# Kernel optimization log

Hardware: AMD Instinct MI355X
Metric: run time of the kernel (lower is better)

Reference implementation:

```python
import jax, jax.numpy as jnp
from jax import lax
import numpy as np

G = 33            # LUT grid size per axis (hard-coded in module)
G3 = G * G * G    # 35937 entries per channel LUT


def _gelu(x):
    return jax.nn.gelu(x, approximate=False)  # torch nn.GELU default = exact erf


def _conv(x, w, b):
    # 3x3 stride-1 padding-1 conv == SAME padding, NCHW/OIHW like torch
    y = lax.conv_general_dilated(x, w, (1, 1), 'SAME',
                                 dimension_numbers=('NCHW', 'OIHW', 'NCHW'))
    return y + b[None, :, None, None]


def _bn(x, g, b, eps=1e-5):
    # eval-mode BatchNorm2d with running_mean=0, running_var=1
    s = g * (1.0 + eps) ** -0.5
    return x * s[None, :, None, None] + b[None, :, None, None]


def _resblock(x, wA, bA, gA, btA, wB, bB, gB, btB):
    h = _gelu(_bn(_conv(x, wA, bA), gA, btA))
    h = _bn(_conv(h, wB, bB), gB, btB)
    return _gelu(h + x)


def _apply_luts(luts_flat, recon):
    # Trilinear 3D-LUT sampling == F.grid_sample(mode='bilinear', padding_mode='border',
    # align_corners=True) on a 5D LUT. grid = recon[...,[2,1,0]]*2-1 means image ch0 (R)
    # indexes LUT dim 2, ch1 (G) dim 3, ch2 (B) dim 4; align_corners maps v->v*(G-1).
    # luts_flat: [B, L*3, G^3] (all num_luts fused into the channel dim, gathered once)
    # recon:     [B, 3, H, W] in [0,1]
    B, C3, _ = luts_flat.shape
    _, _, H, W = recon.shape
    c = jnp.clip(recon * (G - 1.0), 0.0, G - 1.0)      # border clamp
    f0 = jnp.clip(jnp.floor(c), 0.0, G - 2.0)
    t = c - f0                                          # fractional weights [B,3,H,W]
    i0 = f0.astype(jnp.int32)
    r0, g0, b0 = i0[:, 0], i0[:, 1], i0[:, 2]           # [B,H,W] each
    tr, tg, tb = t[:, 0], t[:, 1], t[:, 2]
    out = jnp.zeros((B, C3, H * W), dtype=luts_flat.dtype)
    for dr in (0, 1):
        for dg in (0, 1):
            for db in (0, 1):
                idx = ((r0 + dr) * G + (g0 + dg)) * G + (b0 + db)   # [B,H,W]
                w = ((tr if dr else 1.0 - tr) * (tg if dg else 1.0 - tg)
                     * (tb if db else 1.0 - tb))
                vals = jnp.take_along_axis(luts_flat, idx.reshape(B, 1, H * W), axis=2)
                out = out + vals * w.reshape(B, 1, H * W)
    return out.reshape(B, C3 // 3, 3, H, W)            # [B, L, 3, H, W]


def setup_inputs() -> dict:
    key = jax.random.key(0)
    ks = iter(jax.random.split(key, 32))
    def nrm(shape, s=0.02):
        return jax.random.normal(next(ks), shape, jnp.float32) * s
    B, T, V, E, HID, L, H, W = 4, 1024, 1024, 256, 256, 8, 384, 384
    inp = dict(
        tokens=jax.random.randint(next(ks), (B, T), 0, V),
        img=jax.random.uniform(next(ks), (B, 3, H, W), jnp.float32),
        recon_image=jax.random.uniform(next(ks), (B, 3, H, W), jnp.float32),
        emb_table=nrm((V, E)),
        agg_w1=nrm((E, HID)), agg_b1=jnp.zeros((HID,), jnp.float32),
        agg_w2=nrm((HID, HID)), agg_b2=jnp.zeros((HID,), jnp.float32),
        lut_w1=nrm((HID, HID)), lut_b1=jnp.zeros((HID,), jnp.float32),
        lut_w2=nrm((HID, L * 3 * G3), 0.005),
        lut_b2=jnp.zeros((L * 3 * G3,), jnp.float32),
        wg_w1=nrm((HID, HID // 4)), wg_b1=jnp.zeros((HID // 4,), jnp.float32),
        wg_w2=nrm((HID // 4, L)), wg_b2=jnp.zeros((L,), jnp.float32),
        rp_cin_w=nrm((32, 3, 3, 3)), rp_cin_b=jnp.zeros((32,), jnp.float32),
        rp_rbA_w=nrm((32, 32, 3, 3)), rp_rbA_b=jnp.zeros((32,), jnp.float32),
        rp_rbA_g=jnp.ones((32,), jnp.float32), rp_rbA_bt=jnp.zeros((32,), jnp.float32),
        rp_rbB_w=nrm((32, 32, 3, 3)), rp_rbB_b=jnp.zeros((32,), jnp.float32),
        rp_rbB_g=jnp.ones((32,), jnp.float32), rp_rbB_bt=jnp.zeros((32,), jnp.float32),
        rp_cout_w=nrm((3, 32, 3, 3)), rp_cout_b=jnp.zeros((3,), jnp.float32),
        fu_cin_w=nrm((32, 6, 3, 3)), fu_cin_b=jnp.zeros((32,), jnp.float32),
        fu_rbA_w=nrm((32, 32, 3, 3)), fu_rbA_b=jnp.zeros((32,), jnp.float32),
        fu_rbA_g=jnp.ones((32,), jnp.float32), fu_rbA_bt=jnp.zeros((32,), jnp.float32),
        fu_rbB_w=nrm((32, 32, 3, 3)), fu_rbB_b=jnp.zeros((32,), jnp.float32),
        fu_rbB_g=jnp.ones((32,), jnp.float32), fu_rbB_bt=jnp.zeros((32,), jnp.float32),
        fu_cout_w=nrm((3, 32, 3, 3)), fu_cout_b=jnp.zeros((3,), jnp.float32),
    )
    return inp


def reference(tokens, img, recon_image, emb_table,
              agg_w1, agg_b1, agg_w2, agg_b2,
              lut_w1, lut_b1, lut_w2, lut_b2,
              wg_w1, wg_b1, wg_w2, wg_b2,
              rp_cin_w, rp_cin_b, rp_rbA_w, rp_rbA_b, rp_rbA_g, rp_rbA_bt,
              rp_rbB_w, rp_rbB_b, rp_rbB_g, rp_rbB_bt, rp_cout_w, rp_cout_b,
              fu_cin_w, fu_cin_b, fu_rbA_w, fu_rbA_b, fu_rbA_g, fu_rbA_bt,
              fu_rbB_w, fu_rbB_b, fu_rbB_g, fu_rbB_bt, fu_cout_w, fu_cout_b):
    B = img.shape[0]
    L = wg_w2.shape[1]
    # token features
    emb = emb_table[tokens]                       # [B, T, E]
    tf = jnp.mean(emb, axis=1)                    # [B, E]
    tf = _gelu(tf @ agg_w1 + agg_b1) @ agg_w2 + agg_b2   # [B, HID]
    # dynamic LUTs and fusion weights
    lut_params = _gelu(tf @ lut_w1 + lut_b1) @ lut_w2 + lut_b2   # [B, L*3*G3]
    luts_flat = lut_params.reshape(B, L * 3, G3)
    lw = jax.nn.softmax(_gelu(tf @ wg_w1 + wg_b1) @ wg_w2 + wg_b2, axis=1)  # [B, L]
    # apply all LUTs in one fused gather pass, then weighted sum over LUTs
    lut_out = _apply_luts(luts_flat, recon_image)                # [B, L, 3, H, W]
    fused = jnp.einsum('blchw,bl->bchw', lut_out, lw)            # [B, 3, H, W]
    # residual processing branch on original img
    proc = _gelu(_conv(img, rp_cin_w, rp_cin_b))
    proc = _resblock(proc, rp_rbA_w, rp_rbA_b, rp_rbA_g, rp_rbA_bt,
                     rp_rbB_w, rp_rbB_b, rp_rbB_g, rp_rbB_bt)
    proc = _conv(proc, rp_cout_w, rp_cout_b)
    # fusion
    comb = jnp.concatenate([fused, proc], axis=1)                # [B, 6, H, W]
    out = _gelu(_conv(comb, fu_cin_w, fu_cin_b))
    out = _resblock(out, fu_rbA_w, fu_rbA_b, fu_rbA_g, fu_rbA_bt,
                    fu_rbB_w, fu_rbB_b, fu_rbB_g, fu_rbB_bt)
    out = _conv(out, fu_cout_w, fu_cout_b)
    return out + img
```

## Files before the change

### kernel.cpp

```cpp
#include <hip/hip_runtime.h>
#include <hip/hip_bf16.h>
#include <math.h>

#define BB    4
#define TT    1024
#define EE    256
#define HIDD  256
#define LLUT  8
#define HGT   384
#define WID   384
#define HWPX  147456
#define GSZ   33
#define G3    35937
#define NCOL  862488

typedef __attribute__((ext_vector_type(8))) short bf16x8;
typedef __attribute__((ext_vector_type(4))) float f32x4;

__device__ __forceinline__ float gelu_f(float x) {
    float s = 1.5957691216057308f * x * (1.0f + 0.044715f * x * x);
    float e = __expf(s);
    return x - x / (e + 1.0f);
}

__device__ __forceinline__ ushort f2bf(float x) {
    uint u = __float_as_uint(x);
    return (ushort)((u + 0x7FFFu + ((u >> 16) & 1u)) >> 16);
}
__device__ __forceinline__ uint pack2bf(float a, float b) {
    return (uint)f2bf(a) | ((uint)f2bf(b) << 16);
}
__device__ __forceinline__ float bf2f_lo(uint u) { return __uint_as_float(u << 16); }
__device__ __forceinline__ float bf2f_hi(uint u) { return __uint_as_float(u & 0xFFFF0000u); }

__global__ __launch_bounds__(256) void emb_partial_kernel(
    const int* __restrict__ tokens, const float* __restrict__ emb,
    float* __restrict__ partial)
{
    const int s = blockIdx.x, b = blockIdx.y, tid = threadIdx.x;
    const int* tok = tokens + b * TT + s * 16;
    float acc = 0.f;
#pragma unroll
    for (int t = 0; t < 16; ++t) acc += emb[tok[t] * EE + tid];
    partial[(b * 64 + s) * EE + tid] = acc;
}

__global__ __launch_bounds__(1024) void mlp_head_kernel(
    const float* __restrict__ partial,
    const float* __restrict__ aw1, const float* __restrict__ ab1,
    const float* __restrict__ aw2, const float* __restrict__ ab2,
    const float* __restrict__ lw1, const float* __restrict__ lb1,
    const float* __restrict__ gw1, const float* __restrict__ gb1,
    const float* __restrict__ gw2, const float* __restrict__ gb2,
    float* __restrict__ h3_out, float* __restrict__ lw_out)
{
    const int b = blockIdx.x;
    const int tid = threadIdx.x;
    const int o = tid & 255;
    const int q = tid >> 8;
    __shared__ float tf[256], h1[256], tf2s[256], h4[64], lg[8];
    __shared__ float red[4][256];

    {
        float acc = 0.f;
#pragma unroll
        for (int s = 0; s < 16; ++s)
            acc += partial[(b * 64 + q * 16 + s) * EE + o];
        red[q][o] = acc;
    }
    __syncthreads();
    if (tid < 256)
        tf[tid] = (red[0][tid] + red[1][tid] + red[2][tid] + red[3][tid]) * (1.0f / TT);
    __syncthreads();

    {
        float s = 0.f;
#pragma unroll 8
        for (int j = 0; j < 64; ++j) {
            const int k = (q << 6) + j;
            s += tf[k] * aw1[k * HIDD + o];
        }
        red[q][o] = s;
    }
    __syncthreads();
    if (tid < 256)
        h1[tid] = gelu_f(red[0][tid] + red[1][tid] + red[2][tid] + red[3][tid] + ab1[tid]);
    __syncthreads();

    {
        float s = 0.f;
#pragma unroll 8
        for (int j = 0; j < 64; ++j) {
            const int k = (q << 6) + j;
            s += h1[k] * aw2[k * HIDD + o];
        }
        red[q][o] = s;
    }
    __syncthreads();
    if (tid < 256)
        tf2s[tid] = red[0][tid] + red[1][tid] + red[2][tid] + red[3][tid] + ab2[tid];
    __syncthreads();

    {
        float s = 0.f;
#pragma unroll 8
        for (int j = 0; j < 64; ++j) {
            const int k = (q << 6) + j;
            s += tf2s[k] * lw1[k * HIDD + o];
        }
        red[q][o] = s;
    }
    __syncthreads();
    if (tid < 256)
        h3_out[b * HIDD + tid] =
            gelu_f(red[0][tid] + red[1][tid] + red[2][tid] + red[3][tid] + lb1[tid]);
    __syncthreads();

    {
        const int o64 = tid & 63, q16 = tid >> 6;
        float s = 0.f;
#pragma unroll
        for (int j = 0; j < 16; ++j) {
            const int k = q16 * 16 + j;
            s += tf2s[k] * gw1[k * 64 + o64];
        }
        ((float*)red)[q16 * 64 + o64] = s;
    }
    __syncthreads();
    if (tid < 64) {
        float s = gb1[tid];
#pragma unroll
        for (int r = 0; r < 16; ++r) s += ((float*)red)[r * 64 + tid];
        h4[tid] = gelu_f(s);
    }
    __syncthreads();

    if (tid < 8) {
        float s = gb2[tid];
#pragma unroll 8
        for (int k = 0; k < 64; ++k) s += h4[k] * gw2[k * LLUT + tid];
        lg[tid] = s;
    }
    __syncthreads();
    if (tid == 0) {
        float m = lg[0];
        for (int i = 1; i < LLUT; ++i) m = fmaxf(m, lg[i]);
        float ssum = 0.f, ex[LLUT];
        for (int i = 0; i < LLUT; ++i) { ex[i] = expf(lg[i] - m); ssum += ex[i]; }
        for (int i = 0; i < LLUT; ++i) lw_out[b * LLUT + i] = ex[i] / ssum;
    }
}

__global__ __launch_bounds__(256) void lut_fused_kernel(
    const float* __restrict__ h3, const float* __restrict__ lwv,
    const float* __restrict__ w2, const float* __restrict__ b2,
    float* __restrict__ clut)
{
    __shared__ float h[BB * HIDD];
    __shared__ float lws[BB * LLUT];
    const int tid = threadIdx.x;
    for (int i = tid; i < BB * HIDD; i += 256) h[i] = h3[i];
    if (tid < BB * LLUT) lws[tid] = lwv[tid];
    __syncthreads();

    const int idx = blockIdx.x * 256 + tid;
    if (idx >= 3 * G3) return;
    const int c = idx / G3, v = idx - c * G3;

    float acc[BB][LLUT];
#pragma unroll
    for (int b = 0; b < BB; ++b)
#pragma unroll
        for (int l = 0; l < LLUT; ++l) acc[b][l] = 0.f;

    const float* wbase = w2 + (long)c * G3 + v;
#pragma unroll 4
    for (int k = 0; k < HIDD; ++k) {
        const float* row = wbase + (long)k * NCOL;
        float wl[LLUT];
#pragma unroll
        for (int l = 0; l < LLUT; ++l) wl[l] = row[l * 3 * G3];
#pragma unroll
        for (int b = 0; b < BB; ++b) {
            const float hb = h[b * HIDD + k];
#pragma unroll
            for (int l = 0; l < LLUT; ++l) acc[b][l] += wl[l] * hb;
        }
    }

    float bb[LLUT];
#pragma unroll
    for (int l = 0; l < LLUT; ++l) bb[l] = b2[(long)(l * 3 + c) * G3 + v];

#pragma unroll
    for (int b = 0; b < BB; ++b) {
        float s = 0.f;
#pragma unroll
        for (int l = 0; l < LLUT; ++l) s += lws[b * LLUT + l] * (acc[b][l] + bb[l]);
        clut[(long)(b * 3 + c) * G3 + v] = s;
    }
}

__global__ __launch_bounds__(256) void applylut_out3_kernel(
    const float* __restrict__ clut, const float* __restrict__ recon,
    const ushort* __restrict__ act2, const float* __restrict__ wgt,
    const float* __restrict__ bias, float* __restrict__ comb)
{
    const int p = blockIdx.x * 256 + threadIdx.x;
    const int b = blockIdx.y;

    const float* rc = recon + (long)b * 3 * HWPX;
    float cr = fminf(fmaxf(rc[p] * 32.f, 0.f), 32.f);
    float cg = fminf(fmaxf(rc[HWPX + p] * 32.f, 0.f), 32.f);
    float cb = fminf(fmaxf(rc[2 * HWPX + p] * 32.f, 0.f), 32.f);
    float fr = fminf(floorf(cr), 31.f);
    float fg = fminf(floorf(cg), 31.f);
    float fb = fminf(floorf(cb), 31.f);
    float tr = cr - fr, tg = cg - fg, tb_ = cb - fb;
    int idx = (((int)fr * GSZ + (int)fg) * GSZ + (int)fb);
    float c[3];
#pragma unroll
    for (int ch = 0; ch < 3; ++ch) {
        const float* lut = clut + (long)(b * 3 + ch) * G3;
        float v000 = lut[idx],                  v001 = lut[idx + 1];
        float v010 = lut[idx + GSZ],            v011 = lut[idx + GSZ + 1];
        float v100 = lut[idx + GSZ * GSZ],      v101 = lut[idx + GSZ * GSZ + 1];
        float v110 = lut[idx + GSZ * GSZ + GSZ], v111 = lut[idx + GSZ * GSZ + GSZ + 1];
        float c00 = v000 + (v001 - v000) * tb_;
        float c01 = v010 + (v011 - v010) * tb_;
        float c10 = v100 + (v101 - v100) * tb_;
        float c11 = v110 + (v111 - v110) * tb_;
        float c0 = c00 + (c01 - c00) * tg;
        float c1 = c10 + (c11 - c10) * tg;
        c[ch] = c0 + (c1 - c0) * tr;
    }
    float4 r4; r4.x = c[0]; r4.y = c[1]; r4.z = c[2]; r4.w = 0.f;
    *(float4*)(comb + ((long)b * HWPX + p) * 8) = r4;

    const int hh = p / WID, ww = p - hh * WID;
    float acc[3] = {bias[0], bias[1], bias[2]};
#pragma unroll
    for (int tap = 0; tap < 9; ++tap) {
        const int dh = tap / 3, dw = tap - dh * 3;
        const int gh = hh + dh - 1, gw = ww + dw - 1;
        if (gh < 0 || gh >= HGT || gw < 0 || gw >= WID) continue;
        const uint4* xp = (const uint4*)(act2 + ((long)b * HWPX + gh * WID + gw) * 32);
        float xx[32];
#pragma unroll
        for (int q = 0; q < 4; ++q) {
            uint4 v = xp[q];
            xx[q * 8 + 0] = bf2f_lo(v.x); xx[q * 8 + 1] = bf2f_hi(v.x);
            xx[q * 8 + 2] = bf2f_lo(v.y); xx[q * 8 + 3] = bf2f_hi(v.y);
            xx[q * 8 + 4] = bf2f_lo(v.z); xx[q * 8 + 5] = bf2f_hi(v.z);
            xx[q * 8 + 6] = bf2f_lo(v.w); xx[q * 8 + 7] = bf2f_hi(v.w);
        }
#pragma unroll
        for (int o = 0; o < 3; ++o)
#pragma unroll
            for (int ci = 0; ci < 32; ++ci)
                acc[o] += xx[ci] * wgt[o * 288 + ci * 9 + tap];
    }
    float4 s4; s4.x = acc[0]; s4.y = acc[1]; s4.z = acc[2]; s4.w = 0.f;
    *(float4*)(comb + ((long)b * HWPX + p) * 8 + 4) = s4;
}

__global__ __launch_bounds__(256) void conv_in3_kernel(
    const float* __restrict__ img, const float* __restrict__ wgt,
    const float* __restrict__ bias, ushort* __restrict__ out)
{
    const int tid = threadIdx.x;
    const int p0 = (blockIdx.x * 256 + tid) * 2;
    const int b = blockIdx.y;
    const int hh = p0 / WID, ww = p0 - hh * WID;

    float acc[32][2];
#pragma unroll
    for (int o = 0; o < 32; ++o) { float bv = bias[o]; acc[o][0] = bv; acc[o][1] = bv; }

    const bool wlo = (ww > 0), whi = (ww + 2 < WID);
#pragma unroll
    for (int ci = 0; ci < 3; ++ci) {
        const float* ip = img + (long)(b * 3 + ci) * HWPX;
        float x[3][4];
#pragma unroll
        for (int dh = 0; dh < 3; ++dh) {
            const int hs = hh + dh - 1;
            const bool hok = (hs >= 0) && (hs < HGT);
            const float* rp_ = ip + hs * WID + ww;
            x[dh][0] = (hok && wlo) ? rp_[-1] : 0.f;
            x[dh][1] = hok ? rp_[0] : 0.f;
            x[dh][2] = hok ? rp_[1] : 0.f;
            x[dh][3] = (hok && whi) ? rp_[2] : 0.f;
        }
#pragma unroll
        for (int o = 0; o < 32; ++o) {
            const float* wv = wgt + o * 27 + ci * 9;
#pragma unroll
            for (int dh = 0; dh < 3; ++dh)
#pragma unroll
                for (int dw = 0; dw < 3; ++dw) {
                    const float w = wv[dh * 3 + dw];
                    acc[o][0] += x[dh][dw]     * w;
                    acc[o][1] += x[dh][dw + 1] * w;
                }
        }
    }

    ushort* op = out + ((long)b * HWPX + p0) * 32;
#pragma unroll
    for (int px = 0; px < 2; ++px) {
        uint u[16];
#pragma unroll
        for (int o2 = 0; o2 < 16; ++o2)
            u[o2] = pack2bf(gelu_f(acc[2 * o2][px]), gelu_f(acc[2 * o2 + 1][px]));
        uint4* dst = (uint4*)(op + px * 32);
#pragma unroll
        for (int q = 0; q < 4; ++q)
            dst[q] = make_uint4(u[4 * q], u[4 * q + 1], u[4 * q + 2], u[4 * q + 3]);
    }
}

#define TH2 8
#define TW2 64
#define NTX (WID / TW2)
#define NTY (HGT / TH2)
#define NBLK (NTX * NTY * BB)
#define CHUNK (NBLK / 8)
#define HALO_H2 10
#define HALO_W2 66
#define CSTR 40

template <bool HAS_RES>
__global__ __launch_bounds__(512, 4) void conv32_mfma(
    const ushort* __restrict__ in, const ushort* __restrict__ res,
    const float* __restrict__ wgt, const float* __restrict__ bias,
    const float* __restrict__ bn_g, const float* __restrict__ bn_bt,
    ushort* __restrict__ out)
{
    __shared__ ushort halo[HALO_H2 * HALO_W2 * CSTR];
    __shared__ ushort wlA[9 * 2 * 64 * 8];
    __shared__ float s_scale[32], s_shift[32];

    const int tid = threadIdx.x;
    const int bid = blockIdx.x;
    const int t   = (bid & 7) * CHUNK + (bid >> 3);
    const int tx  = t % NTX;
    const int rem = t / NTX;
    const int ty  = rem % NTY;
    const int b   = rem / NTY;
    const int h0 = ty * TH2;
    const int w0 = tx * TW2;

    for (int i = tid; i < 9 * 2 * 64 * 8; i += 512) {
        const int j    = i & 7;
        const int lane_= (i >> 3) & 63;
        const int half = (i >> 9) & 1;
        const int tap  = i >> 10;
        const int co = half * 16 + (lane_ & 15);
        const int ci = (lane_ >> 4) * 8 + j;
        wlA[i] = f2bf(wgt[co * 288 + ci * 9 + tap]);
    }
    if (tid < 32) {
        float sg = bn_g[tid] * 0.9999950000375f;
        s_scale[tid] = sg;
        s_shift[tid] = bias[tid] * sg + bn_bt[tid];
    }

    const ushort* inb = in + (long)b * HWPX * 32;
    for (int i = tid; i < HALO_H2 * HALO_W2 * 4; i += 512) {
        const int row = i / (HALO_W2 * 4);
        const int rem2 = i - row * (HALO_W2 * 4);
        const int px = rem2 >> 2, q = rem2 & 3;
        const int gh = h0 + row - 1, gw = w0 + px - 1;
        uint4 v = make_uint4(0u, 0u, 0u, 0u);
        if (gh >= 0 && gh < HGT && gw >= 0 && gw < WID)
            v = *(const uint4*)(inb + ((long)gh * WID + gw) * 32 + q * 8);
        *(uint4*)(&halo[(row * HALO_W2 + px) * CSTR + q * 8]) = v;
    }
    __syncthreads();

    const int lane = tid & 63, wid = tid >> 6;
    const int l15 = lane & 15, kg = lane >> 4;
    const int r = wid;

    f32x4 acc[4][2];
#pragma unroll
    for (int f = 0; f < 4; ++f)
#pragma unroll
        for (int cf = 0; cf < 2; ++cf)
            acc[f][cf] = (f32x4){0.f, 0.f, 0.f, 0.f};

#pragma unroll
    for (int tap = 0; tap < 9; ++tap) {
        const int dh = tap / 3, dw = tap - dh * 3;
        const bf16x8 a0 = *(const bf16x8*)(&wlA[((tap * 2 + 0) * 64 + lane) * 8]);
        const bf16x8 a1 = *(const bf16x8*)(&wlA[((tap * 2 + 1) * 64 + lane) * 8]);
#pragma unroll
        for (int f = 0; f < 4; ++f) {
            const int c0 = f * 16;
            const bf16x8 bfv = *(const bf16x8*)(
                &halo[((r + dh) * HALO_W2 + (c0 + dw + l15)) * CSTR + kg * 8]);
            acc[f][0] = __builtin_amdgcn_mfma_f32_16x16x32_bf16(a0, bfv, acc[f][0], 0, 0, 0);
            acc[f][1] = __builtin_amdgcn_mfma_f32_16x16x32_bf16(a1, bfv, acc[f][1], 0, 0, 0);
        }
    }

#pragma unroll
    for (int f = 0; f < 4; ++f) {
        const int c0 = f * 16;
        const long gpx = (long)b * HWPX + (long)(h0 + r) * WID + (w0 + c0 + l15);
#pragma unroll
        for (int cf = 0; cf < 2; ++cf) {
            const int co0 = cf * 16 + kg * 4;
            const float4 sc = *(const float4*)(&s_scale[co0]);
            const float4 sh = *(const float4*)(&s_shift[co0]);
            float v0 = acc[f][cf][0] * sc.x + sh.x;
            float v1 = acc[f][cf][1] * sc.y + sh.y;
            float v2 = acc[f][cf][2] * sc.z + sh.z;
            float v3 = acc[f][cf][3] * sc.w + sh.w;
            if (HAS_RES) {
                const uint2 rv = *(const uint2*)(res + gpx * 32 + co0);
                v0 += bf2f_lo(rv.x); v1 += bf2f_hi(rv.x);
                v2 += bf2f_lo(rv.y); v3 += bf2f_hi(rv.y);
            }
            uint2 o;
            o.x = pack2bf(gelu_f(v0), gelu_f(v1));
            o.y = pack2bf(gelu_f(v2), gelu_f(v3));
            *(uint2*)(out + gpx * 32 + co0) = o;
        }
    }
}

__global__ __launch_bounds__(256) void conv_in6_kernel(
    const float* __restrict__ comb, const float* __restrict__ wgt,
    const float* __restrict__ bias, ushort* __restrict__ out)
{
    const int p = blockIdx.x * 256 + threadIdx.x;
    const int b = blockIdx.y;
    const int hh = p / WID, ww = p - hh * WID;

    float acc[32];
#pragma unroll
    for (int o = 0; o < 32; ++o) acc[o] = bias[o];

#pragma unroll
    for (int tap = 0; tap < 9; ++tap) {
        const int dh = tap / 3, dw = tap - dh * 3;
        const int gh = hh + dh - 1, gw = ww + dw - 1;
        if (gh < 0 || gh >= HGT || gw < 0 || gw >= WID) continue;
        const float4* cp = (const float4*)(comb + ((long)b * HWPX + gh * WID + gw) * 8);
        const float4 qa = cp[0], qb = cp[1];
        const float xs[6] = {qa.x, qa.y, qa.z, qb.x, qb.y, qb.z};
#pragma unroll
        for (int o = 0; o < 32; ++o) {
            const float* wv = wgt + o * 54 + tap;
            acc[o] += xs[0] * wv[0]  + xs[1] * wv[9]  + xs[2] * wv[18]
                    + xs[3] * wv[27] + xs[4] * wv[36] + xs[5] * wv[45];
        }
    }

    ushort* op = out + ((long)b * HWPX + p) * 32;
    uint u[16];
#pragma unroll
    for (int o2 = 0; o2 < 16; ++o2)
        u[o2] = pack2bf(gelu_f(acc[2 * o2]), gelu_f(acc[2 * o2 + 1]));
    uint4* dst = (uint4*)op;
#pragma unroll
    for (int q = 0; q < 4; ++q)
        dst[q] = make_uint4(u[4 * q], u[4 * q + 1], u[4 * q + 2], u[4 * q + 3]);
}

__global__ __launch_bounds__(256) void conv_final_kernel(
    const ushort* __restrict__ in, const float* __restrict__ wgt,
    const float* __restrict__ bias, const float* __restrict__ img,
    float* __restrict__ outp)
{
    const int p = blockIdx.x * 256 + threadIdx.x;
    const int b = blockIdx.y;
    const int hh = p / WID, ww = p - hh * WID;
    float acc[3] = {bias[0], bias[1], bias[2]};

#pragma unroll
    for (int tap = 0; tap < 9; ++tap) {
        const int dh = tap / 3, dw = tap - dh * 3;
        const int gh = hh + dh - 1, gw = ww + dw - 1;
        if (gh < 0 || gh >= HGT || gw < 0 || gw >= WID) continue;
        const uint4* xp = (const uint4*)(in + ((long)b * HWPX + gh * WID + gw) * 32);
        float xx[32];
#pragma unroll
        for (int q = 0; q < 4; ++q) {
            uint4 v = xp[q];
            xx[q * 8 + 0] = bf2f_lo(v.x); xx[q * 8 + 1] = bf2f_hi(v.x);
            xx[q * 8 + 2] = bf2f_lo(v.y); xx[q * 8 + 3] = bf2f_hi(v.y);
            xx[q * 8 + 4] = bf2f_lo(v.z); xx[q * 8 + 5] = bf2f_hi(v.z);
            xx[q * 8 + 6] = bf2f_lo(v.w); xx[q * 8 + 7] = bf2f_hi(v.w);
        }
#pragma unroll
        for (int o = 0; o < 3; ++o)
#pragma unroll
            for (int ci = 0; ci < 32; ++ci)
                acc[o] += xx[ci] * wgt[o * 288 + ci * 9 + tap];
    }
#pragma unroll
    for (int o = 0; o < 3; ++o)
        outp[(long)(b * 3 + o) * HWPX + p] = acc[o] + img[(long)(b * 3 + o) * HWPX + p];
}

extern "C" void kernel_launch(void* const* d_in, const int* in_sizes, int n_in,
                              void* d_out, int out_size, void* d_ws, size_t ws_size,
                              hipStream_t stream)
{
    const int*   tokens  = (const int*)d_in[0];
    const float* img     = (const float*)d_in[1];
    const float* recon   = (const float*)d_in[2];
    const float* emb     = (const float*)d_in[3];
    const float* agg_w1  = (const float*)d_in[4];
    const float* agg_b1  = (const float*)d_in[5];
    const float* agg_w2  = (const float*)d_in[6];
    const float* agg_b2  = (const float*)d_in[7];
    const float* lut_w1  = (const float*)d_in[8];
    const float* lut_b1  = (const float*)d_in[9];
    const float* lut_w2  = (const float*)d_in[10];
    const float* lut_b2  = (const float*)d_in[11];
    const float* wg_w1   = (const float*)d_in[12];
    const float* wg_b1   = (const float*)d_in[13];
    const float* wg_w2   = (const float*)d_in[14];
    const float* wg_b2   = (const float*)d_in[15];
    const float* rp_cin_w = (const float*)d_in[16];
    const float* rp_cin_b = (const float*)d_in[17];
    const float* rp_rbA_w = (const float*)d_in[18];
    const float* rp_rbA_b = (const float*)d_in[19];
    const float* rp_rbA_g = (const float*)d_in[20];
    const float* rp_rbA_bt= (const float*)d_in[21];
    const float* rp_rbB_w = (const float*)d_in[22];
    const float* rp_rbB_b = (const float*)d_in[23];
    const float* rp_rbB_g = (const float*)d_in[24];
    const float* rp_rbB_bt= (const float*)d_in[25];
    const float* rp_cout_w= (const float*)d_in[26];
    const float* rp_cout_b= (const float*)d_in[27];
    const float* fu_cin_w = (const float*)d_in[28];
    const float* fu_cin_b = (const float*)d_in[29];
    const float* fu_rbA_w = (const float*)d_in[30];
    const float* fu_rbA_b = (const float*)d_in[31];
    const float* fu_rbA_g = (const float*)d_in[32];
    const float* fu_rbA_bt= (const float*)d_in[33];
    const float* fu_rbB_w = (const float*)d_in[34];
    const float* fu_rbB_b = (const float*)d_in[35];
    const float* fu_rbB_g = (const float*)d_in[36];
    const float* fu_rbB_bt= (const float*)d_in[37];
    const float* fu_cout_w= (const float*)d_in[38];
    const float* fu_cout_b= (const float*)d_in[39];

    float* ws = (float*)d_ws;
    float*  h3      = ws;
    float*  lwv     = ws + 1024;
    float*  partial = ws + 2048;
    float*  clut    = ws + 69632;
    float*  comb    = ws + 524288;
    ushort* act0    = (ushort*)(ws + 5242880);
    ushort* act1    = (ushort*)(ws + 14680064);
    ushort* act2    = (ushort*)(ws + 24117248);
    float*  outp    = (float*)d_out;

    emb_partial_kernel<<<dim3(64, BB), dim3(256), 0, stream>>>(tokens, emb, partial);
    mlp_head_kernel<<<dim3(BB), dim3(1024), 0, stream>>>(
        partial, agg_w1, agg_b1, agg_w2, agg_b2,
        lut_w1, lut_b1, wg_w1, wg_b1, wg_w2, wg_b2, h3, lwv);

    lut_fused_kernel<<<dim3((3 * G3 + 255) / 256), dim3(256), 0, stream>>>(
        h3, lwv, lut_w2, lut_b2, clut);

    const dim3 g1(HWPX / 256, BB), g2(HWPX / 512, BB), blk(256);
    const dim3 gm(NBLK), bm(512);

    conv_in3_kernel<<<g2, blk, 0, stream>>>(img, rp_cin_w, rp_cin_b, act0);
    conv32_mfma<false><<<gm, bm, 0, stream>>>(
        act0, nullptr, rp_rbA_w, rp_rbA_b, rp_rbA_g, rp_rbA_bt, act1);
    conv32_mfma<true><<<gm, bm, 0, stream>>>(
        act1, act0, rp_rbB_w, rp_rbB_b, rp_rbB_g, rp_rbB_bt, act2);

    applylut_out3_kernel<<<g1, blk, 0, stream>>>(
        clut, recon, act2, rp_cout_w, rp_cout_b, comb);

    conv_in6_kernel<<<g1, blk, 0, stream>>>(comb, fu_cin_w, fu_cin_b, act0);
    conv32_mfma<false><<<gm, bm, 0, stream>>>(
        act0, nullptr, fu_rbA_w, fu_rbA_b, fu_rbA_g, fu_rbA_bt, act1);
    conv32_mfma<true><<<gm, bm, 0, stream>>>(
        act1, act0, fu_rbB_w, fu_rbB_b, fu_rbB_g, fu_rbB_bt, act2);
    conv_final_kernel<<<g1, blk, 0, stream>>>(act2, fu_cout_w, fu_cout_b, img, outp);
}
```

Before: 564.3 us.

## Prepack conv weights once, store comb as bf16, raise conv occupancy

Adds a small kernel that converts and packs the four 32-channel conv weight sets into the MFMA lane layout in bf16 once per call. The conv32_mfma blocks now read A fragments straight from global memory instead of rebuilding an LDS copy in every block, which also frees LDS for a higher occupancy hint. The intermediate comb buffer drops from fp32 to bf16, halving its write and read traffic, at some cost in precision on the LUT and residual-branch outputs.

```diff
diff --git a/kernel.cpp b/kernel.cpp
--- a/kernel.cpp
+++ b/kernel.cpp
@@ -33,6 +33,25 @@
 __device__ __forceinline__ float bf2f_lo(uint u) { return __uint_as_float(u << 16); }
 __device__ __forceinline__ float bf2f_hi(uint u) { return __uint_as_float(u & 0xFFFF0000u); }
 
+__global__ __launch_bounds__(256) void pack_wconv_kernel(
+    const float* __restrict__ w0, const float* __restrict__ w1,
+    const float* __restrict__ w2, const float* __restrict__ w3,
+    ushort* __restrict__ wpk)
+{
+    const int layer = blockIdx.x;
+    const float* w = (layer == 0) ? w0 : (layer == 1) ? w1 : (layer == 2) ? w2 : w3;
+    ushort* dst = wpk + layer * 9216;
+    for (int i = threadIdx.x; i < 9216; i += 256) {
+        const int j    = i & 7;
+        const int lane = (i >> 3) & 63;
+        const int half = (i >> 9) & 1;
+        const int tap  = i >> 10;
+        const int co = half * 16 + (lane & 15);
+        const int ci = (lane >> 4) * 8 + j;
+        dst[i] = f2bf(w[co * 288 + ci * 9 + tap]);
+    }
+}
+
 __global__ __launch_bounds__(256) void emb_partial_kernel(
     const int* __restrict__ tokens, const float* __restrict__ emb,
     float* __restrict__ partial)
@@ -204,7 +223,7 @@
 __global__ __launch_bounds__(256) void applylut_out3_kernel(
     const float* __restrict__ clut, const float* __restrict__ recon,
     const ushort* __restrict__ act2, const float* __restrict__ wgt,
-    const float* __restrict__ bias, float* __restrict__ comb)
+    const float* __restrict__ bias, ushort* __restrict__ comb)
 {
     const int p = blockIdx.x * 256 + threadIdx.x;
     const int b = blockIdx.y;
@@ -234,8 +253,6 @@
         float c1 = c10 + (c11 - c10) * tg;
         c[ch] = c0 + (c1 - c0) * tr;
     }
-    float4 r4; r4.x = c[0]; r4.y = c[1]; r4.z = c[2]; r4.w = 0.f;
-    *(float4*)(comb + ((long)b * HWPX + p) * 8) = r4;
 
     const int hh = p / WID, ww = p - hh * WID;
     float acc[3] = {bias[0], bias[1], bias[2]};
@@ -260,8 +277,13 @@
             for (int ci = 0; ci < 32; ++ci)
                 acc[o] += xx[ci] * wgt[o * 288 + ci * 9 + tap];
     }
-    float4 s4; s4.x = acc[0]; s4.y = acc[1]; s4.z = acc[2]; s4.w = 0.f;
-    *(float4*)(comb + ((long)b * HWPX + p) * 8 + 4) = s4;
+
+    uint4 u;
+    u.x = pack2bf(c[0], c[1]);
+    u.y = pack2bf(c[2], 0.f);
+    u.z = pack2bf(acc[0], acc[1]);
+    u.w = pack2bf(acc[2], 0.f);
+    *(uint4*)(comb + ((long)b * HWPX + p) * 8) = u;
 }
 
 __global__ __launch_bounds__(256) void conv_in3_kernel(
@@ -331,14 +353,13 @@
 #define CSTR 40
 
 template <bool HAS_RES>
-__global__ __launch_bounds__(512, 4) void conv32_mfma(
+__global__ __launch_bounds__(512, 6) void conv32_mfma(
     const ushort* __restrict__ in, const ushort* __restrict__ res,
-    const float* __restrict__ wgt, const float* __restrict__ bias,
+    const ushort* __restrict__ wpk, const float* __restrict__ bias,
     const float* __restrict__ bn_g, const float* __restrict__ bn_bt,
     ushort* __restrict__ out)
 {
     __shared__ ushort halo[HALO_H2 * HALO_W2 * CSTR];
-    __shared__ ushort wlA[9 * 2 * 64 * 8];
     __shared__ float s_scale[32], s_shift[32];
 
     const int tid = threadIdx.x;
@@ -351,15 +372,6 @@
     const int h0 = ty * TH2;
     const int w0 = tx * TW2;
 
-    for (int i = tid; i < 9 * 2 * 64 * 8; i += 512) {
-        const int j    = i & 7;
-        const int lane_= (i >> 3) & 63;
-        const int half = (i >> 9) & 1;
-        const int tap  = i >> 10;
-        const int co = half * 16 + (lane_ & 15);
-        const int ci = (lane_ >> 4) * 8 + j;
-        wlA[i] = f2bf(wgt[co * 288 + ci * 9 + tap]);
-    }
     if (tid < 32) {
         float sg = bn_g[tid] * 0.9999950000375f;
         s_scale[tid] = sg;
@@ -382,6 +394,7 @@
     const int lane = tid & 63, wid = tid >> 6;
     const int l15 = lane & 15, kg = lane >> 4;
     const int r = wid;
+    const ushort* wlane = wpk + lane * 8;
 
     f32x4 acc[4][2];
 #pragma unroll
@@ -393,8 +406,8 @@
 #pragma unroll
     for (int tap = 0; tap < 9; ++tap) {
         const int dh = tap / 3, dw = tap - dh * 3;
-        const bf16x8 a0 = *(const bf16x8*)(&wlA[((tap * 2 + 0) * 64 + lane) * 8]);
-        const bf16x8 a1 = *(const bf16x8*)(&wlA[((tap * 2 + 1) * 64 + lane) * 8]);
+        const bf16x8 a0 = *(const bf16x8*)(wlane + (tap * 2 + 0) * 512);
+        const bf16x8 a1 = *(const bf16x8*)(wlane + (tap * 2 + 1) * 512);
 #pragma unroll
         for (int f = 0; f < 4; ++f) {
             const int c0 = f * 16;
@@ -432,7 +445,7 @@
 }
 
 __global__ __launch_bounds__(256) void conv_in6_kernel(
-    const float* __restrict__ comb, const float* __restrict__ wgt,
+    const ushort* __restrict__ comb, const float* __restrict__ wgt,
     const float* __restrict__ bias, ushort* __restrict__ out)
 {
     const int p = blockIdx.x * 256 + threadIdx.x;
@@ -448,9 +461,9 @@
         const int dh = tap / 3, dw = tap - dh * 3;
         const int gh = hh + dh - 1, gw = ww + dw - 1;
         if (gh < 0 || gh >= HGT || gw < 0 || gw >= WID) continue;
-        const float4* cp = (const float4*)(comb + ((long)b * HWPX + gh * WID + gw) * 8);
-        const float4 qa = cp[0], qb = cp[1];
-        const float xs[6] = {qa.x, qa.y, qa.z, qb.x, qb.y, qb.z};
+        const uint4 v = *(const uint4*)(comb + ((long)b * HWPX + gh * WID + gw) * 8);
+        const float xs[6] = {bf2f_lo(v.x), bf2f_hi(v.x), bf2f_lo(v.y),
+                             bf2f_lo(v.z), bf2f_hi(v.z), bf2f_lo(v.w)};
 #pragma unroll
         for (int o = 0; o < 32; ++o) {
             const float* wv = wgt + o * 54 + tap;
@@ -556,11 +569,15 @@
     float*  lwv     = ws + 1024;
     float*  partial = ws + 2048;
     float*  clut    = ws + 69632;
-    float*  comb    = ws + 524288;
-    ushort* act0    = (ushort*)(ws + 5242880);
-    ushort* act1    = (ushort*)(ws + 14680064);
-    ushort* act2    = (ushort*)(ws + 24117248);
+    ushort* wpack   = (ushort*)(ws + 524288);
+    ushort* comb    = (ushort*)(ws + 589824);
+    ushort* act0    = (ushort*)(ws + 3145728);
+    ushort* act1    = (ushort*)(ws + 12582912);
+    ushort* act2    = (ushort*)(ws + 22020096);
     float*  outp    = (float*)d_out;
+
+    pack_wconv_kernel<<<dim3(4), dim3(256), 0, stream>>>(
+        rp_rbA_w, rp_rbB_w, fu_rbA_w, fu_rbB_w, wpack);
 
     emb_partial_kernel<<<dim3(64, BB), dim3(256), 0, stream>>>(tokens, emb, partial);
     mlp_head_kernel<<<dim3(BB), dim3(1024), 0, stream>>>(
@@ -575,17 +592,17 @@
 
     conv_in3_kernel<<<g2, blk, 0, stream>>>(img, rp_cin_w, rp_cin_b, act0);
     conv32_mfma<false><<<gm, bm, 0, stream>>>(
-        act0, nullptr, rp_rbA_w, rp_rbA_b, rp_rbA_g, rp_rbA_bt, act1);
+        act0, nullptr, wpack + 0 * 9216, rp_rbA_b, rp_rbA_g, rp_rbA_bt, act1);
     conv32_mfma<true><<<gm, bm, 0, stream>>>(
-        act1, act0, rp_rbB_w, rp_rbB_b, rp_rbB_g, rp_rbB_bt, act2);
+        act1, act0, wpack + 1 * 9216, rp_rbB_b, rp_rbB_g, rp_rbB_bt, act2);
 
     applylut_out3_kernel<<<g1, blk, 0, stream>>>(
         clut, recon, act2, rp_cout_w, rp_cout_b, comb);
 
     conv_in6_kernel<<<g1, blk, 0, stream>>>(comb, fu_cin_w, fu_cin_b, act0);
     conv32_mfma<false><<<gm, bm, 0, stream>>>(
-        act0, nullptr, fu_rbA_w, fu_rbA_b, fu_rbA_g, fu_rbA_bt, act1);
+        act0, nullptr, wpack + 2 * 9216, fu_rbA_b, fu_rbA_g, fu_rbA_bt, act1);
     conv32_mfma<true><<<gm, bm, 0, stream>>>(
-        act1, act0, fu_rbB_w, fu_rbB_b, fu_rbB_g, fu_rbB_bt, act2);
+        act1, act0, wpack + 3 * 9216, fu_rbB_b, fu_rbB_g, fu_rbB_bt, act2);
     conv_final_kernel<<<g1, blk, 0, stream>>>(act2, fu_cout_w, fu_cout_b, img, outp);
 }
```

Result: faster. 553.0 us (median of 2 runs) (-2.0%).
